# Optimization experiments

Hardware: AMD Instinct MI355X
Metric: run time of the kernel (lower is better)

Reference implementation:

```python
import jax, jax.numpy as jnp
import numpy as np

B, T_ENC, ENC, DEC, MEL = 32, 1024, 1024, 1024, 80


def setup_inputs() -> dict:
    key = jax.random.key(0)
    ks = jax.random.split(key, 10)
    s = lambda k, shape, sc=1.0: (jax.random.normal(k, shape, dtype=jnp.float32) * sc)
    return {
        "prev_mel_frame": s(ks[0], (B, MEL)),
        "encoder_outputs": s(ks[1], (B, T_ENC, ENC)),
        "h": s(ks[2], (B, DEC)),
        "c": s(ks[3], (B, DEC)),
        # AdditiveAttention learned scale vector (use_scale=True default)
        "attn_scale": s(ks[4], (ENC,), 0.05),
        # LSTMCell params: input dim = MEL + ENC, gates order i, f, c, o (Keras)
        "kernel": s(ks[5], (MEL + ENC, 4 * DEC), 0.02),
        "rec_kernel": s(ks[6], (DEC, 4 * DEC), 0.02),
        "bias": s(ks[7], (4 * DEC,), 0.02),
        # Dense projection to mel
        "proj_w": s(ks[8], (DEC, MEL), 0.02),
        "proj_b": s(ks[9], (MEL,), 0.02),
    }


def reference(prev_mel_frame, encoder_outputs, h, c,
              attn_scale, kernel, rec_kernel, bias, proj_w, proj_b):
    # Additive (Bahdanau) attention: scores[b,t] = sum_d scale_d * tanh(h[b,d] + enc[b,t,d])
    feat = jnp.tanh(h[:, None, :] + encoder_outputs)          # [B, T, D]
    scores = jnp.einsum("btd,d->bt", feat, attn_scale)         # [B, T]
    attn = jax.nn.softmax(scores, axis=-1)
    context = jnp.einsum("bt,btd->bd", attn, encoder_outputs)  # [B, ENC]

    # LSTMCell step on concat([prev_mel, context])
    x = jnp.concatenate([prev_mel_frame, context], axis=-1)    # [B, MEL+ENC]
    z = x @ kernel + h @ rec_kernel + bias                     # [B, 4*DEC]
    i, f, g, o = jnp.split(z, 4, axis=-1)
    i = jax.nn.sigmoid(i)
    f = jax.nn.sigmoid(f)
    o = jax.nn.sigmoid(o)
    c_new = f * c + i * jnp.tanh(g)
    h_new = o * jnp.tanh(c_new)

    mel_frame = h_new @ proj_w + proj_b                        # [B, MEL]
    return mel_frame, h_new, c_new
```

## Files before the change

kernel.cpp:

```cpp
#include <hip/hip_runtime.h>

#define BB 32
#define TT 1024
#define ENCD 1024
#define DECD 1024
#define MELD 80
#define KTOT (MELD + ENCD + DECD)
#define NZ (4 * DECD)
#define KCH 128
#define KC 17
#define NTT 32

__device__ float g_cp[NTT * BB * ENCD];
__device__ float g_m[NTT * BB];
__device__ float g_s[NTT * BB];
__device__ float g_ctx[BB * ENCD];
__device__ float g_zp[KC * BB * NZ];
__device__ float g_hn[BB * DECD];

__device__ __forceinline__ float tanh_fast(float x) {
    return 1.f - __fdividef(2.f, __expf(2.f * x) + 1.f);
}
__device__ __forceinline__ float sigmoid_fast(float x) {
    return __fdividef(1.f, 1.f + __expf(-x));
}

__global__ __launch_bounds__(256, 4) void k_attn(const float* __restrict__ enc,
                                                 const float* __restrict__ hst,
                                                 const float* __restrict__ scale) {
    int b = blockIdx.x, tc = blockIdx.y;
    int w = threadIdx.x >> 6, lane = threadIdx.x & 63;
    const float4* hp = (const float4*)(hst + (size_t)b * DECD);
    const float4* sp = (const float4*)scale;
    float4 hr0 = hp[lane], hr1 = hp[lane + 64], hr2 = hp[lane + 128], hr3 = hp[lane + 192];
    float4 sr0 = sp[lane], sr1 = sp[lane + 64], sr2 = sp[lane + 128], sr3 = sp[lane + 192];

    float m = -1e30f, s = 0.f;
    float4 c0 = {0.f, 0.f, 0.f, 0.f}, c1 = c0, c2 = c0, c3 = c0;

    const float4* ep = (const float4*)(enc + ((size_t)b * TT + tc * 32 + w * 8) * ENCD) + lane;
#pragma unroll 2
    for (int t = 0; t < 8; t++) {
        float4 e0 = ep[t * 256];
        float4 e1 = ep[t * 256 + 64];
        float4 e2 = ep[t * 256 + 128];
        float4 e3 = ep[t * 256 + 192];
        float sc = 0.f;
        sc = fmaf(sr0.x, tanh_fast(hr0.x + e0.x), sc);
        sc = fmaf(sr0.y, tanh_fast(hr0.y + e0.y), sc);
        sc = fmaf(sr0.z, tanh_fast(hr0.z + e0.z), sc);
        sc = fmaf(sr0.w, tanh_fast(hr0.w + e0.w), sc);
        sc = fmaf(sr1.x, tanh_fast(hr1.x + e1.x), sc);
        sc = fmaf(sr1.y, tanh_fast(hr1.y + e1.y), sc);
        sc = fmaf(sr1.z, tanh_fast(hr1.z + e1.z), sc);
        sc = fmaf(sr1.w, tanh_fast(hr1.w + e1.w), sc);
        sc = fmaf(sr2.x, tanh_fast(hr2.x + e2.x), sc);
        sc = fmaf(sr2.y, tanh_fast(hr2.y + e2.y), sc);
        sc = fmaf(sr2.z, tanh_fast(hr2.z + e2.z), sc);
        sc = fmaf(sr2.w, tanh_fast(hr2.w + e2.w), sc);
        sc = fmaf(sr3.x, tanh_fast(hr3.x + e3.x), sc);
        sc = fmaf(sr3.y, tanh_fast(hr3.y + e3.y), sc);
        sc = fmaf(sr3.z, tanh_fast(hr3.z + e3.z), sc);
        sc = fmaf(sr3.w, tanh_fast(hr3.w + e3.w), sc);
#pragma unroll
        for (int off = 32; off; off >>= 1) sc += __shfl_xor(sc, off, 64);
        float mn = fmaxf(m, sc);
        float al = __expf(m - mn);
        float p  = __expf(sc - mn);
        m = mn;
        s = fmaf(s, al, p);
        c0.x = fmaf(p, e0.x, c0.x * al); c0.y = fmaf(p, e0.y, c0.y * al);
        c0.z = fmaf(p, e0.z, c0.z * al); c0.w = fmaf(p, e0.w, c0.w * al);
        c1.x = fmaf(p, e1.x, c1.x * al); c1.y = fmaf(p, e1.y, c1.y * al);
        c1.z = fmaf(p, e1.z, c1.z * al); c1.w = fmaf(p, e1.w, c1.w * al);
        c2.x = fmaf(p, e2.x, c2.x * al); c2.y = fmaf(p, e2.y, c2.y * al);
        c2.z = fmaf(p, e2.z, c2.z * al); c2.w = fmaf(p, e2.w, c2.w * al);
        c3.x = fmaf(p, e3.x, c3.x * al); c3.y = fmaf(p, e3.y, c3.y * al);
        c3.z = fmaf(p, e3.z, c3.z * al); c3.w = fmaf(p, e3.w, c3.w * al);
    }

    __shared__ float lm[4], ls[4];
    __shared__ float4 lctx[4][256];
    if (lane == 0) { lm[w] = m; ls[w] = s; }
    __syncthreads();
    float M = fmaxf(fmaxf(lm[0], lm[1]), fmaxf(lm[2], lm[3]));
    float S = ls[0] * __expf(lm[0] - M) + ls[1] * __expf(lm[1] - M) +
              ls[2] * __expf(lm[2] - M) + ls[3] * __expf(lm[3] - M);
    float be = __expf(m - M);
    float4 o;
    o.x = c0.x * be; o.y = c0.y * be; o.z = c0.z * be; o.w = c0.w * be;
    lctx[w][lane] = o;
    o.x = c1.x * be; o.y = c1.y * be; o.z = c1.z * be; o.w = c1.w * be;
    lctx[w][lane + 64] = o;
    o.x = c2.x * be; o.y = c2.y * be; o.z = c2.z * be; o.w = c2.w * be;
    lctx[w][lane + 128] = o;
    o.x = c3.x * be; o.y = c3.y * be; o.z = c3.z * be; o.w = c3.w * be;
    lctx[w][lane + 192] = o;
    __syncthreads();
    int tid = threadIdx.x;
    float4 a0 = lctx[0][tid], a1 = lctx[1][tid], a2 = lctx[2][tid], a3 = lctx[3][tid];
    float4 r;
    r.x = (a0.x + a1.x) + (a2.x + a3.x);
    r.y = (a0.y + a1.y) + (a2.y + a3.y);
    r.z = (a0.z + a1.z) + (a2.z + a3.z);
    r.w = (a0.w + a1.w) + (a2.w + a3.w);
    ((float4*)g_cp)[((size_t)tc * BB + b) * (ENCD / 4) + tid] = r;
    if (tid == 0) { g_m[tc * BB + b] = M; g_s[tc * BB + b] = S; }
}

__global__ __launch_bounds__(256) void k_combine() {
    __shared__ float wgt[NTT];
    int b = blockIdx.x, dq = blockIdx.y, tid = threadIdx.x;
    float M = -1e30f;
#pragma unroll
    for (int tt = 0; tt < NTT; tt++) M = fmaxf(M, g_m[tt * BB + b]);
    float S = 0.f;
#pragma unroll
    for (int tt = 0; tt < NTT; tt++) S += g_s[tt * BB + b] * __expf(g_m[tt * BB + b] - M);
    if (tid < NTT) wgt[tid] = __expf(g_m[tid * BB + b] - M) * __fdividef(1.f, S);
    __syncthreads();
    int d = dq * 256 + tid;
    float acc = 0.f;
#pragma unroll 8
    for (int tt = 0; tt < NTT; tt++)
        acc = fmaf(wgt[tt], g_cp[((size_t)tt * BB + b) * ENCD + d], acc);
    g_ctx[b * ENCD + d] = acc;
}

__global__ __launch_bounds__(256) void k_zmm(const float* __restrict__ pm,
                                             const float* __restrict__ h,
                                             const float* __restrict__ kern,
                                             const float* __restrict__ reck) {
    __shared__ float xs[KCH * 32];
    int jt = blockIdx.x & 15, kc = blockIdx.x >> 4;
    int k0 = kc * KCH;
    int kcount = min(KCH, KTOT - k0);
    int tid = threadIdx.x;
    for (int idx = tid; idx < kcount * 32; idx += 256) {
        int kk = idx >> 5, b = idx & 31;
        int k = k0 + kk;
        float v;
        if (k < MELD)             v = pm[b * MELD + k];
        else if (k < MELD + ENCD) v = g_ctx[b * ENCD + (k - MELD)];
        else                      v = h[b * DECD + (k - MELD - ENCD)];
        xs[idx] = v;
    }
    __syncthreads();
    int j = jt * 256 + tid;
    float acc[32];
#pragma unroll
    for (int b = 0; b < 32; b++) acc[b] = 0.f;
    for (int kk0 = 0; kk0 < kcount; kk0 += 8) {
        float w[8];
#pragma unroll
        for (int i = 0; i < 8; i++) {
            int k = k0 + kk0 + i;
            w[i] = (k < MELD + ENCD) ? kern[(size_t)k * NZ + j]
                                     : reck[(size_t)(k - MELD - ENCD) * NZ + j];
        }
#pragma unroll
        for (int i = 0; i < 8; i++) {
            const float* xr = xs + (kk0 + i) * 32;
#pragma unroll
            for (int b = 0; b < 32; b++) acc[b] = fmaf(xr[b], w[i], acc[b]);
        }
    }
#pragma unroll
    for (int b = 0; b < 32; b++) g_zp[((size_t)kc * BB + b) * NZ + j] = acc[b];
}

__global__ __launch_bounds__(256) void k_gates(const float* __restrict__ bias,
                                               const float* __restrict__ c,
                                               float* __restrict__ out) {
    __shared__ float sacc[4][4][64];
    int b = blockIdx.x >> 4, jq = blockIdx.x & 15;
    int jl = threadIdx.x & 63, grp = threadIdx.x >> 6;
    int j = jq * 64 + jl;
    int kc0 = (grp == 0) ? 0 : grp * 4 + 1;
    int kc1 = grp * 4 + 5;
    float zi = 0.f, zf = 0.f, zg = 0.f, zo = 0.f;
    for (int kc = kc0; kc < kc1; kc++) {
        const float* zp = g_zp + ((size_t)kc * BB + b) * NZ;
        zi += zp[j];
        zf += zp[1024 + j];
        zg += zp[2048 + j];
        zo += zp[3072 + j];
    }
    sacc[grp][0][jl] = zi; sacc[grp][1][jl] = zf;
    sacc[grp][2][jl] = zg; sacc[grp][3][jl] = zo;
    __syncthreads();
    if (grp == 0) {
        zi = sacc[0][0][jl] + sacc[1][0][jl] + sacc[2][0][jl] + sacc[3][0][jl] + bias[j];
        zf = sacc[0][1][jl] + sacc[1][1][jl] + sacc[2][1][jl] + sacc[3][1][jl] + bias[1024 + j];
        zg = sacc[0][2][jl] + sacc[1][2][jl] + sacc[2][2][jl] + sacc[3][2][jl] + bias[2048 + j];
        zo = sacc[0][3][jl] + sacc[1][3][jl] + sacc[2][3][jl] + sacc[3][3][jl] + bias[3072 + j];
        int idx = b * 1024 + j;
        float cn = sigmoid_fast(zf) * c[idx] + sigmoid_fast(zi) * tanh_fast(zg);
        float hn = sigmoid_fast(zo) * tanh_fast(cn);
        g_hn[idx] = hn;
        out[2560 + idx] = hn;
        out[35328 + idx] = cn;
    }
}

__global__ __launch_bounds__(256) void k_proj(const float* __restrict__ pw,
                                              const float* __restrict__ pb,
                                              float* __restrict__ out) {
    __shared__ float lh[1024];
    __shared__ float pacc[2][MELD];
    int b = blockIdx.x, tid = threadIdx.x;
    for (int i = tid; i < 1024; i += 256) lh[i] = g_hn[b * 1024 + i];
    __syncthreads();
    int m = tid & 127;
    int g = tid >> 7;
    if (m < MELD) {
        float acc = 0.f;
        int d0 = g * 512;
#pragma unroll 8
        for (int d = d0; d < d0 + 512; d++) acc = fmaf(lh[d], pw[d * MELD + m], acc);
        pacc[g][m] = acc;
    }
    __syncthreads();
    if (tid < MELD) out[b * MELD + tid] = pacc[0][tid] + pacc[1][tid] + pb[tid];
}

extern "C" void kernel_launch(void* const* d_in, const int* in_sizes, int n_in,
                              void* d_out, int out_size, void* d_ws, size_t ws_size,
                              hipStream_t stream) {
    const float* pm   = (const float*)d_in[0];
    const float* enc  = (const float*)d_in[1];
    const float* h    = (const float*)d_in[2];
    const float* c    = (const float*)d_in[3];
    const float* asc  = (const float*)d_in[4];
    const float* kern = (const float*)d_in[5];
    const float* reck = (const float*)d_in[6];
    const float* bias = (const float*)d_in[7];
    const float* pw   = (const float*)d_in[8];
    const float* pb   = (const float*)d_in[9];
    float* out = (float*)d_out;

    k_attn   <<<dim3(32, NTT), 256, 0, stream>>>(enc, h, asc);
    k_combine<<<dim3(32, 4), 256, 0, stream>>>();
    k_zmm    <<<272, 256, 0, stream>>>(pm, h, kern, reck);
    k_gates  <<<512, 256, 0, stream>>>(bias, c, out);
    k_proj   <<<32, 256, 0, stream>>>(pw, pb, out);
}
```

Baseline: 306.9 us.

## Stage encoder rows in shared memory so context accumulates per-thread

The attention kernel now processes the 32 timesteps in four groups of 8 rows. Each wave scores two rows and writes the raw encoder rows plus their scores to shared memory. After a barrier, every thread applies the group's online-softmax update and accumulates one float4 column of the context across all 8 rows. This removes the 16-register per-wave context accumulators and the final cross-wave shared-memory reduction, which should lower register pressure. In exchange it adds 32KB of shared memory per block, two barriers per group, and extra LDS traffic, and the shared memory may limit occupancy under the 4-blocks launch bound.

```diff
diff --git a/kernel.cpp b/kernel.cpp
--- a/kernel.cpp
+++ b/kernel.cpp
@@ -10,6 +10,7 @@
 #define KCH 128
 #define KC 17
 #define NTT 32
+#define QR 8
 
 __device__ float g_cp[NTT * BB * ENCD];
 __device__ float g_m[NTT * BB];
@@ -28,83 +29,76 @@
 __global__ __launch_bounds__(256, 4) void k_attn(const float* __restrict__ enc,
                                                  const float* __restrict__ hst,
                                                  const float* __restrict__ scale) {
+    __shared__ float es[QR][ENCD];
+    __shared__ float ssc[QR];
     int b = blockIdx.x, tc = blockIdx.y;
-    int w = threadIdx.x >> 6, lane = threadIdx.x & 63;
+    int tid = threadIdx.x, w = tid >> 6, lane = tid & 63;
     const float4* hp = (const float4*)(hst + (size_t)b * DECD);
     const float4* sp = (const float4*)scale;
     float4 hr0 = hp[lane], hr1 = hp[lane + 64], hr2 = hp[lane + 128], hr3 = hp[lane + 192];
     float4 sr0 = sp[lane], sr1 = sp[lane + 64], sr2 = sp[lane + 128], sr3 = sp[lane + 192];
 
-    float m = -1e30f, s = 0.f;
-    float4 c0 = {0.f, 0.f, 0.f, 0.f}, c1 = c0, c2 = c0, c3 = c0;
-
-    const float4* ep = (const float4*)(enc + ((size_t)b * TT + tc * 32 + w * 8) * ENCD) + lane;
-#pragma unroll 2
-    for (int t = 0; t < 8; t++) {
-        float4 e0 = ep[t * 256];
-        float4 e1 = ep[t * 256 + 64];
-        float4 e2 = ep[t * 256 + 128];
-        float4 e3 = ep[t * 256 + 192];
-        float sc = 0.f;
-        sc = fmaf(sr0.x, tanh_fast(hr0.x + e0.x), sc);
-        sc = fmaf(sr0.y, tanh_fast(hr0.y + e0.y), sc);
-        sc = fmaf(sr0.z, tanh_fast(hr0.z + e0.z), sc);
-        sc = fmaf(sr0.w, tanh_fast(hr0.w + e0.w), sc);
-        sc = fmaf(sr1.x, tanh_fast(hr1.x + e1.x), sc);
-        sc = fmaf(sr1.y, tanh_fast(hr1.y + e1.y), sc);
-        sc = fmaf(sr1.z, tanh_fast(hr1.z + e1.z), sc);
-        sc = fmaf(sr1.w, tanh_fast(hr1.w + e1.w), sc);
-        sc = fmaf(sr2.x, tanh_fast(hr2.x + e2.x), sc);
-        sc = fmaf(sr2.y, tanh_fast(hr2.y + e2.y), sc);
-        sc = fmaf(sr2.z, tanh_fast(hr2.z + e2.z), sc);
-        sc = fmaf(sr2.w, tanh_fast(hr2.w + e2.w), sc);
-        sc = fmaf(sr3.x, tanh_fast(hr3.x + e3.x), sc);
-        sc = fmaf(sr3.y, tanh_fast(hr3.y + e3.y), sc);
-        sc = fmaf(sr3.z, tanh_fast(hr3.z + e3.z), sc);
-        sc = fmaf(sr3.w, tanh_fast(hr3.w + e3.w), sc);
-#pragma unroll
-        for (int off = 32; off; off >>= 1) sc += __shfl_xor(sc, off, 64);
-        float mn = fmaxf(m, sc);
-        float al = __expf(m - mn);
-        float p  = __expf(sc - mn);
-        m = mn;
-        s = fmaf(s, al, p);
-        c0.x = fmaf(p, e0.x, c0.x * al); c0.y = fmaf(p, e0.y, c0.y * al);
-        c0.z = fmaf(p, e0.z, c0.z * al); c0.w = fmaf(p, e0.w, c0.w * al);
-        c1.x = fmaf(p, e1.x, c1.x * al); c1.y = fmaf(p, e1.y, c1.y * al);
-        c1.z = fmaf(p, e1.z, c1.z * al); c1.w = fmaf(p, e1.w, c1.w * al);
-        c2.x = fmaf(p, e2.x, c2.x * al); c2.y = fmaf(p, e2.y, c2.y * al);
-        c2.z = fmaf(p, e2.z, c2.z * al); c2.w = fmaf(p, e2.w, c2.w * al);
-        c3.x = fmaf(p, e3.x, c3.x * al); c3.y = fmaf(p, e3.y, c3.y * al);
-        c3.z = fmaf(p, e3.z, c3.z * al); c3.w = fmaf(p, e3.w, c3.w * al);
-    }
-
-    __shared__ float lm[4], ls[4];
-    __shared__ float4 lctx[4][256];
-    if (lane == 0) { lm[w] = m; ls[w] = s; }
-    __syncthreads();
-    float M = fmaxf(fmaxf(lm[0], lm[1]), fmaxf(lm[2], lm[3]));
-    float S = ls[0] * __expf(lm[0] - M) + ls[1] * __expf(lm[1] - M) +
-              ls[2] * __expf(lm[2] - M) + ls[3] * __expf(lm[3] - M);
-    float be = __expf(m - M);
-    float4 o;
-    o.x = c0.x * be; o.y = c0.y * be; o.z = c0.z * be; o.w = c0.w * be;
-    lctx[w][lane] = o;
-    o.x = c1.x * be; o.y = c1.y * be; o.z = c1.z * be; o.w = c1.w * be;
-    lctx[w][lane + 64] = o;
-    o.x = c2.x * be; o.y = c2.y * be; o.z = c2.z * be; o.w = c2.w * be;
-    lctx[w][lane + 128] = o;
-    o.x = c3.x * be; o.y = c3.y * be; o.z = c3.z * be; o.w = c3.w * be;
-    lctx[w][lane + 192] = o;
-    __syncthreads();
-    int tid = threadIdx.x;
-    float4 a0 = lctx[0][tid], a1 = lctx[1][tid], a2 = lctx[2][tid], a3 = lctx[3][tid];
-    float4 r;
-    r.x = (a0.x + a1.x) + (a2.x + a3.x);
-    r.y = (a0.y + a1.y) + (a2.y + a3.y);
-    r.z = (a0.z + a1.z) + (a2.z + a3.z);
-    r.w = (a0.w + a1.w) + (a2.w + a3.w);
-    ((float4*)g_cp)[((size_t)tc * BB + b) * (ENCD / 4) + tid] = r;
+    float M = -1e30f, S = 0.f;
+    float cx = 0.f, cy = 0.f, cz = 0.f, cw = 0.f;
+    const float4* ebase = (const float4*)(enc + ((size_t)b * TT + tc * 32) * ENCD);
+
+    for (int q = 0; q < 4; q++) {
+#pragma unroll
+        for (int rr = 0; rr < 2; rr++) {
+            int r = w * 2 + rr;
+            const float4* ep = ebase + (size_t)(q * QR + r) * (ENCD / 4) + lane;
+            float4 e0 = ep[0], e1 = ep[64], e2 = ep[128], e3 = ep[192];
+            float sc = 0.f;
+            sc = fmaf(sr0.x, tanh_fast(hr0.x + e0.x), sc);
+            sc = fmaf(sr0.y, tanh_fast(hr0.y + e0.y), sc);
+            sc = fmaf(sr0.z, tanh_fast(hr0.z + e0.z), sc);
+            sc = fmaf(sr0.w, tanh_fast(hr0.w + e0.w), sc);
+            sc = fmaf(sr1.x, tanh_fast(hr1.x + e1.x), sc);
+            sc = fmaf(sr1.y, tanh_fast(hr1.y + e1.y), sc);
+            sc = fmaf(sr1.z, tanh_fast(hr1.z + e1.z), sc);
+            sc = fmaf(sr1.w, tanh_fast(hr1.w + e1.w), sc);
+            sc = fmaf(sr2.x, tanh_fast(hr2.x + e2.x), sc);
+            sc = fmaf(sr2.y, tanh_fast(hr2.y + e2.y), sc);
+            sc = fmaf(sr2.z, tanh_fast(hr2.z + e2.z), sc);
+            sc = fmaf(sr2.w, tanh_fast(hr2.w + e2.w), sc);
+            sc = fmaf(sr3.x, tanh_fast(hr3.x + e3.x), sc);
+            sc = fmaf(sr3.y, tanh_fast(hr3.y + e3.y), sc);
+            sc = fmaf(sr3.z, tanh_fast(hr3.z + e3.z), sc);
+            sc = fmaf(sr3.w, tanh_fast(hr3.w + e3.w), sc);
+#pragma unroll
+            for (int off = 32; off; off >>= 1) sc += __shfl_xor(sc, off, 64);
+            float4* esr = (float4*)&es[r][0];
+            esr[lane] = e0; esr[lane + 64] = e1;
+            esr[lane + 128] = e2; esr[lane + 192] = e3;
+            if (lane == 0) ssc[r] = sc;
+        }
+        __syncthreads();
+        float s0 = ssc[0], s1 = ssc[1], s2 = ssc[2], s3 = ssc[3];
+        float s4 = ssc[4], s5 = ssc[5], s6 = ssc[6], s7 = ssc[7];
+        float mq = fmaxf(fmaxf(fmaxf(s0, s1), fmaxf(s2, s3)),
+                         fmaxf(fmaxf(s4, s5), fmaxf(s6, s7)));
+        float Mn = fmaxf(M, mq);
+        float alO = __expf(M - Mn);
+        float w0 = __expf(s0 - Mn), w1 = __expf(s1 - Mn);
+        float w2 = __expf(s2 - Mn), w3 = __expf(s3 - Mn);
+        float w4 = __expf(s4 - Mn), w5 = __expf(s5 - Mn);
+        float w6 = __expf(s6 - Mn), w7 = __expf(s7 - Mn);
+        float Sq = ((w0 + w1) + (w2 + w3)) + ((w4 + w5) + (w6 + w7));
+        S = fmaf(S, alO, Sq);
+        M = Mn;
+        cx *= alO; cy *= alO; cz *= alO; cw *= alO;
+        const float4* col = (const float4*)&es[0][0] + tid;
+        float wr[QR] = {w0, w1, w2, w3, w4, w5, w6, w7};
+#pragma unroll
+        for (int r = 0; r < QR; r++) {
+            float4 e = col[r * 256];
+            cx = fmaf(wr[r], e.x, cx); cy = fmaf(wr[r], e.y, cy);
+            cz = fmaf(wr[r], e.z, cz); cw = fmaf(wr[r], e.w, cw);
+        }
+        __syncthreads();
+    }
+    float4 r4; r4.x = cx; r4.y = cy; r4.z = cz; r4.w = cw;
+    ((float4*)g_cp)[((size_t)tc * BB + b) * (ENCD / 4) + tid] = r4;
     if (tid == 0) { g_m[tc * BB + b] = M; g_s[tc * BB + b] = S; }
 }
 
```

Result: faster. 296.8 us (-3.3%).
